# Performance work log

Hardware: AMD Instinct MI355X
Metric: run time of the kernel (lower is better)

Reference implementation:

```python
import jax, jax.numpy as jnp
import numpy as np
import math

H = 5120        # hidden_size
NH = 32         # num heads
HD = H // NH    # head_dim = 160
B = 1
S = 2048
TRAIN_SEQLEN = 8192
BASE = 10000.0


def _rotary_cos_sin(seq_len):
    # Eval-mode RotaryEmbedding: seq_len clamped to training_seqlen, NTK alpha + mscale (logN) scaling.
    eff = max(seq_len, TRAIN_SEQLEN)
    scale = eff / TRAIN_SEQLEN
    mscale = 1.0 if scale <= 1.0 else 0.1 * math.log(scale) + 1.0
    ntk_alpha = max(2 ** math.ceil(math.log(eff / 4096, 2) + 1) - 1, 1)
    base = BASE * ntk_alpha ** (HD / (HD - 2))
    inv_freq = 1.0 / base ** (np.arange(0, HD, 2, dtype=np.float64) / HD)
    t = np.arange(eff, dtype=np.float64)
    freqs = np.outer(t, inv_freq)              # [eff, HD/2]
    emb = np.concatenate([freqs, freqs], axis=-1)  # [eff, HD]
    cos = (mscale * np.cos(emb))[:seq_len].astype(np.float32)
    sin = (mscale * np.sin(emb))[:seq_len].astype(np.float32)
    return jnp.asarray(cos), jnp.asarray(sin)


def _rotate_half(x):
    x1, x2 = x[..., : HD // 2], x[..., HD // 2 :]
    return jnp.concatenate([-x2, x1], axis=-1)


def setup_inputs() -> dict:
    key = jax.random.key(0)
    ks = jax.random.split(key, 6)
    hidden_states = jax.random.normal(ks[0], (B, S, H), jnp.float32)
    residual = jax.random.normal(ks[1], (B, S, H), jnp.float32)
    # boolean causal mask, True = masked (matches masked_fill semantics)
    attention_mask = jnp.triu(jnp.ones((S, S), dtype=bool), k=1)[None, None]
    Wq = jax.random.normal(ks[2], (H, H), jnp.float32) * 0.02      # query: Linear(h, h, bias=False)
    Wkv = jax.random.normal(ks[3], (2 * H, H), jnp.float32) * 0.02  # key_value: Linear(h, 2h, bias=False)
    Wd = jax.random.normal(ks[4], (H, H), jnp.float32) * 0.02       # dense: Linear(h, h) with bias
    bd = jnp.zeros((H,), jnp.float32)
    return {
        "hidden_states": hidden_states,
        "residual": residual,
        "attention_mask": attention_mask,
        "Wq": Wq,
        "Wkv": Wkv,
        "Wd": Wd,
        "bd": bd,
    }


def reference(hidden_states, residual, attention_mask, Wq, Wkv, Wd, bd):
    b, s, h = hidden_states.shape
    # QKV projections (torch Linear: y = x @ W.T)
    q = jnp.einsum('bsh,oh->bso', hidden_states, Wq).reshape(b, s, NH, HD)
    kv = jnp.einsum('bsh,oh->bso', hidden_states, Wkv).reshape(b, s, NH, 2 * HD)
    k, v = kv[..., :HD], kv[..., HD:]
    # rotary embedding with logN mscale folded into cos/sin
    cos, sin = _rotary_cos_sin(s)               # [s, HD]
    cos = cos[None, :, None, :]
    sin = sin[None, :, None, :]
    q = q * cos + _rotate_half(q) * sin
    k = k * cos + _rotate_half(k) * sin
    inv_norm = 1.0 / math.sqrt(HD)
    scores = jnp.einsum('bqnd,bknd->bnqk', q, k) * inv_norm   # [b, nh, s, s]
    scores = jnp.where(attention_mask, jnp.finfo(scores.dtype).min, scores)
    probs = jax.nn.softmax(scores, axis=-1)
    # attention_dropout p=0.0 -> identity
    ctx = jnp.einsum('bnqk,bknd->bqnd', probs, v).reshape(b, s, h)
    out = ctx @ Wd.T + bd
    # dropout_add with hidden_dropout=0.0 (eval) -> residual + out
    return residual + out
```

## Files before the change

### kernel.cpp

```cpp
#include <hip/hip_runtime.h>
#include <cmath>

typedef unsigned short u16;
typedef unsigned int   u32;

using bf16x8 = __attribute__((ext_vector_type(8))) short;
using f32x4  = __attribute__((ext_vector_type(4))) float;

#define S_LEN 2048
#define NHEAD 32
#define HDIM  160
#define HID   5120
#define NQKV  15360

__device__ __forceinline__ f32x4 mfma16(bf16x8 a, bf16x8 b, f32x4 c) {
  return __builtin_amdgcn_mfma_f32_16x16x32_bf16(a, b, c, 0, 0, 0);
}

__device__ __forceinline__ u16 f2bf(float f) {
  u32 u = __builtin_bit_cast(u32, f);
  u += 0x7FFFu + ((u >> 16) & 1u);
  return (u16)(u >> 16);
}
__device__ __forceinline__ float bf2f(u16 h) {
  u32 u = ((u32)h) << 16;
  return __builtin_bit_cast(float, u);
}

__device__ __forceinline__ void gload16(const void* g, void* l) {
  __builtin_amdgcn_global_load_lds((const __attribute__((address_space(1))) void*)g,
                                   (__attribute__((address_space(3))) void*)l, 16, 0, 0);
}

__global__ void cvt_all_kernel(const float* __restrict__ hs, const float* __restrict__ Wq,
                               const float* __restrict__ Wkv, const float* __restrict__ Wd,
                               u16* __restrict__ Xb, u16* __restrict__ Wqkvb,
                               u16* __restrict__ Wdb) {
  const int n_hs = S_LEN * HID / 8;
  const int n_q  = HID * HID / 8;
  const int n_kv = 2 * HID * HID / 8;
  const int n_d  = HID * HID / 8;
  const int total = n_hs + n_q + n_kv + n_d;
  for (int i = blockIdx.x * 256 + threadIdx.x; i < total; i += gridDim.x * 256) {
    const float* src; u16* dst; int j = i;
    if (j < n_hs)                { src = hs;  dst = Xb; }
    else if ((j -= n_hs) < n_q)  { src = Wq;  dst = Wqkvb; }
    else if ((j -= n_q) < n_kv)  { src = Wkv; dst = Wqkvb + (size_t)HID * HID; }
    else { j -= n_kv;              src = Wd;  dst = Wdb; }
    float4 a = ((const float4*)src)[(size_t)j * 2];
    float4 b = ((const float4*)src)[(size_t)j * 2 + 1];
    uint4 o;
    o.x = (u32)f2bf(a.x) | ((u32)f2bf(a.y) << 16);
    o.y = (u32)f2bf(a.z) | ((u32)f2bf(a.w) << 16);
    o.z = (u32)f2bf(b.x) | ((u32)f2bf(b.y) << 16);
    o.w = (u32)f2bf(b.z) | ((u32)f2bf(b.w) << 16);
    ((uint4*)dst)[j] = o;
  }
}

__global__ void rope_table_kernel(float2* __restrict__ tab) {
  __shared__ double invf_s[80];
  int tid = threadIdx.x;
  if (tid < 80) {
    double base = 10000.0 * pow(3.0, 160.0 / 158.0);
    invf_s[tid] = pow(base, -((double)(2 * tid)) / 160.0);
  }
  __syncthreads();
  for (int i = blockIdx.x * 256 + tid; i < S_LEN * 80; i += gridDim.x * 256) {
    int s = i / 80, j = i % 80;
    double ang = fmod((double)s * invf_s[j], 6.283185307179586476925287);
    float a = (float)ang;
    tab[i] = make_float2(cosf(a), sinf(a));
  }
}

__global__ void rope_apply2_kernel(const u16* __restrict__ qkv, const float2* __restrict__ tab,
                                   u16* __restrict__ Qr, u16* __restrict__ Kr) {
  const int n = S_LEN * NHEAD * 80;
  int i = blockIdx.x * 256 + threadIdx.x;
  bool isK = i >= n;
  if (isK) i -= n;
  const u16* src = qkv + (isK ? HID : 0);
  int headStride = isK ? 2 * HDIM : HDIM;
  u16* dst = isK ? Kr : Qr;

  int dp = i % 80; int sh = i / 80; int h = sh % NHEAD; int s = sh / NHEAD;
  int d = 2 * dp;
  const u16* row = src + (size_t)s * NQKV + h * headStride;
  u32 q01 = *(const u32*)&row[d];
  u32 p01 = *(const u32*)&row[d < 80 ? d + 80 : d - 80];
  int j = (d < 80) ? d : d - 80;
  float2 cs0 = tab[s * 80 + j];
  float2 cs1 = tab[s * 80 + j + 1];
  float q0 = bf2f((u16)(q01 & 0xffff)), q1 = bf2f((u16)(q01 >> 16));
  float p0 = bf2f((u16)(p01 & 0xffff)), p1 = bf2f((u16)(p01 >> 16));
  float sgn = (d < 80) ? -1.f : 1.f;
  float o0 = q0 * cs0.x + sgn * p0 * cs0.y;
  float o1 = q1 * cs1.x + sgn * p1 * cs1.y;
  u32 o = (u32)f2bf(o0) | ((u32)f2bf(o1) << 16);
  *(u32*)&dst[((size_t)h * S_LEN + s) * HDIM + d] = o;
}

__global__ void vtrans_kernel(const u16* __restrict__ src, u16* __restrict__ Vt, int rowStride) {
  __shared__ u16 T[HDIM][72];
  int h = blockIdx.y; int s0 = blockIdx.x * 64; int tid = threadIdx.x;
  for (int i = tid; i < 64 * 80; i += 256) {
    int s = i / 80, dp = i % 80;
    u32 v = *(const u32*)&src[(size_t)(s0 + s) * rowStride + h * 320 + 2 * dp];
    T[2 * dp][s]     = (u16)(v & 0xffff);
    T[2 * dp + 1][s] = (u16)(v >> 16);
  }
  __syncthreads();
  for (int i = tid; i < HDIM * 32; i += 256) {
    int d = i / 32, sp = i % 32;
    u32 v = (u32)T[d][2 * sp] | ((u32)T[d][2 * sp + 1] << 16);
    *(u32*)&Vt[((size_t)h * HDIM + d) * S_LEN + s0 + 2 * sp] = v;
  }
}

template<int EPI>
__global__ __launch_bounds__(512, 2) void gemm256(
    const u16* __restrict__ A, const u16* __restrict__ Bm, void* __restrict__ Cout,
    int M, int N, int K, const float* __restrict__ bias, const float* __restrict__ resid)
{
  __shared__ u16 As[2][2][8192];
  __shared__ u16 Bs[2][2][8192];
  int tid = threadIdx.x;
  int w = tid >> 6, l = tid & 63, l15 = l & 15, l4 = l >> 4;
  int wr = w >> 2, wc = w & 3;

  int nbx = gridDim.x;
  int nwg = nbx * gridDim.y;
  int lin = blockIdx.y * nbx + blockIdx.x;
  int cpx = nwg >> 3;
  int swz = (lin & 7) * cpx + (lin >> 3);
  int bm = (swz / nbx) * 256, bn = (swz % nbx) * 256;

  int srow = tid >> 2;
  int scol = ((tid & 3) * 8) ^ ((srow & 8) ? 16 : 0);
  const u16* gAr = A  + (size_t)(bm + srow) * K + scol;
  const u16* gBr = Bm + (size_t)(bn + srow) * K + scol;
  int w512 = w * 512;

  f32x4 acc[8][4];
#pragma unroll
  for (int i = 0; i < 8; i++)
#pragma unroll
    for (int j = 0; j < 4; j++) acc[i][j] = f32x4{0.f, 0.f, 0.f, 0.f};

  int cA = (l4 * 8) ^ ((l15 & 8) ? 16 : 0);
  const int NT = K >> 6;
  int arow = wr * 128;
  int brow = (wc >> 1) * 128 + (wc & 1) * 64;

  auto STA = [&](int kt, int kk) { int p = kt & 1, ko = (kt << 6) + (kk << 5);
    gload16(gAr + ko, &As[p][kk][w512]);
    gload16(gAr + (size_t)128 * K + ko, &As[p][kk][4096 + w512]); };
  auto STB = [&](int kt, int kk) { int p = kt & 1, ko = (kt << 6) + (kk << 5);
    gload16(gBr + ko, &Bs[p][kk][w512]);
    gload16(gBr + (size_t)128 * K + ko, &Bs[p][kk][4096 + w512]); };

  STB(0, 0); STA(0, 0); STB(0, 1); STA(0, 1);
  if (NT > 1) { STB(1, 0); STA(1, 0); STB(1, 1); }
  asm volatile("s_waitcnt vmcnt(6)" ::: "memory");
  __builtin_amdgcn_s_barrier();

  for (int kt = 0; kt < NT; ++kt) {
    int p = kt & 1;
    bf16x8 aF[4], bF0[4], bF1[4];

    if (kt + 1 < NT) STA(kt + 1, 1);
#pragma unroll
    for (int mi = 0; mi < 4; ++mi)
      aF[mi] = *(const bf16x8*)&As[p][0][(arow + mi * 16 + l15) * 32 + cA];
#pragma unroll
    for (int ni = 0; ni < 4; ++ni)
      bF0[ni] = *(const bf16x8*)&Bs[p][0][(brow + ni * 16 + l15) * 32 + cA];
    __builtin_amdgcn_s_barrier();
    __builtin_amdgcn_s_setprio(1);
#pragma unroll
    for (int mi = 0; mi < 4; ++mi)
#pragma unroll
      for (int ni = 0; ni < 4; ++ni)
        acc[mi][ni] = mfma16(aF[mi], bF0[ni], acc[mi][ni]);
    __builtin_amdgcn_s_setprio(0);
    __builtin_amdgcn_s_barrier();

    if (kt + 2 < NT) STB(kt + 2, 0);
#pragma unroll
    for (int mi = 0; mi < 4; ++mi)
      aF[mi] = *(const bf16x8*)&As[p][0][(arow + 64 + mi * 16 + l15) * 32 + cA];
    __builtin_amdgcn_s_barrier();
    __builtin_amdgcn_s_setprio(1);
#pragma unroll
    for (int mi = 0; mi < 4; ++mi)
#pragma unroll
      for (int ni = 0; ni < 4; ++ni)
        acc[4 + mi][ni] = mfma16(aF[mi], bF0[ni], acc[4 + mi][ni]);
    __builtin_amdgcn_s_setprio(0);
    __builtin_amdgcn_s_barrier();

    if (kt + 2 < NT) STA(kt + 2, 0);
#pragma unroll
    for (int mi = 0; mi < 4; ++mi)
      aF[mi] = *(const bf16x8*)&As[p][1][(arow + mi * 16 + l15) * 32 + cA];
#pragma unroll
    for (int ni = 0; ni < 4; ++ni)
      bF1[ni] = *(const bf16x8*)&Bs[p][1][(brow + ni * 16 + l15) * 32 + cA];
    __builtin_amdgcn_s_barrier();
    __builtin_amdgcn_s_setprio(1);
#pragma unroll
    for (int mi = 0; mi < 4; ++mi)
#pragma unroll
      for (int ni = 0; ni < 4; ++ni)
        acc[mi][ni] = mfma16(aF[mi], bF1[ni], acc[mi][ni]);
    __builtin_amdgcn_s_setprio(0);
    __builtin_amdgcn_s_barrier();

    if (kt + 2 < NT) STB(kt + 2, 1);
#pragma unroll
    for (int mi = 0; mi < 4; ++mi)
      aF[mi] = *(const bf16x8*)&As[p][1][(arow + 64 + mi * 16 + l15) * 32 + cA];
    __builtin_amdgcn_s_barrier();
    __builtin_amdgcn_s_setprio(1);
#pragma unroll
    for (int mi = 0; mi < 4; ++mi)
#pragma unroll
      for (int ni = 0; ni < 4; ++ni)
        acc[4 + mi][ni] = mfma16(aF[mi], bF1[ni], acc[4 + mi][ni]);
    __builtin_amdgcn_s_setprio(0);
    if (kt + 2 < NT)      asm volatile("s_waitcnt vmcnt(6)" ::: "memory");
    else if (kt + 1 < NT) asm volatile("s_waitcnt vmcnt(0)" ::: "memory");
    __builtin_amdgcn_s_barrier();
  }

#pragma unroll
  for (int mi = 0; mi < 8; ++mi)
#pragma unroll
    for (int ni = 0; ni < 4; ++ni) {
      int row0 = bm + wr * 128 + mi * 16 + l4 * 4;
      int col  = bn + wc * 64 + ni * 16 + l15;
      if (EPI == 0) {
        u16* C = (u16*)Cout;
#pragma unroll
        for (int r = 0; r < 4; r++) C[(size_t)(row0 + r) * N + col] = f2bf(acc[mi][ni][r]);
      } else {
        float* C = (float*)Cout;
        float b = bias[col];
#pragma unroll
        for (int r = 0; r < 4; r++) {
          size_t idx = (size_t)(row0 + r) * N + col;
          C[idx] = acc[mi][ni][r] + b + resid[idx];
        }
      }
    }
}

template<int EPI>
__global__ __launch_bounds__(256, 2) void gemm_bt(
    const u16* __restrict__ A, const u16* __restrict__ Bm, void* __restrict__ Cout,
    int M, int N, int K, const float* __restrict__ bias, const float* __restrict__ resid)
{
  int tid = threadIdx.x;
  int wv = tid >> 6, l = tid & 63, l15 = l & 15, l4 = l >> 4;
  int nbx = gridDim.x;
  int nwg = nbx * gridDim.y;
  int lin = blockIdx.y * nbx + blockIdx.x;
  int cpx = nwg >> 3;
  int swz = (lin & 7) * cpx + (lin >> 3);
  int bm = (swz / nbx) * 128, bn = (swz % nbx) * 128;

  __shared__ u16 As[128 * 32], Bs[128 * 32];
  f32x4 acc[4][4];
#pragma unroll
  for (int i = 0; i < 4; i++)
#pragma unroll
    for (int j = 0; j < 4; j++) acc[i][j] = f32x4{0.f, 0.f, 0.f, 0.f};

  int wm = (wv >> 1) * 64, wn = (wv & 1) * 64;
  const u16* gA = A + (size_t)(bm + (tid >> 2)) * K + (tid & 3) * 8;
  const u16* gB = Bm + (size_t)(bn + (tid >> 2)) * K + (tid & 3) * 8;
  u16* ldsA = As + wv * 16 * 32;
  u16* ldsB = Bs + wv * 16 * 32;

  for (int k0 = 0; k0 < K; k0 += 32) {
    __syncthreads();
    gload16(gA + k0, ldsA);
    gload16(gA + (size_t)64 * K + k0, ldsA + 64 * 32);
    gload16(gB + k0, ldsB);
    gload16(gB + (size_t)64 * K + k0, ldsB + 64 * 32);
    __syncthreads();
    bf16x8 af[4], bfr[4];
#pragma unroll
    for (int i = 0; i < 4; i++) af[i] = *(const bf16x8*)&As[(wm + i * 16 + l15) * 32 + l4 * 8];
#pragma unroll
    for (int i = 0; i < 4; i++) bfr[i] = *(const bf16x8*)&Bs[(wn + i * 16 + l15) * 32 + l4 * 8];
#pragma unroll
    for (int mi = 0; mi < 4; mi++)
#pragma unroll
      for (int ni = 0; ni < 4; ni++) acc[mi][ni] = mfma16(af[mi], bfr[ni], acc[mi][ni]);
  }

#pragma unroll
  for (int mi = 0; mi < 4; mi++)
#pragma unroll
    for (int ni = 0; ni < 4; ni++) {
      int row0 = bm + wm + mi * 16 + l4 * 4;
      int col  = bn + wn + ni * 16 + l15;
      if (EPI == 0) {
        u16* C = (u16*)Cout;
#pragma unroll
        for (int r = 0; r < 4; r++) C[(size_t)(row0 + r) * N + col] = f2bf(acc[mi][ni][r]);
      } else {
        float* C = (float*)Cout;
        float b = bias[col];
#pragma unroll
        for (int r = 0; r < 4; r++) {
          size_t idx = (size_t)(row0 + r) * N + col;
          C[idx] = acc[mi][ni][r] + b + resid[idx];
        }
      }
    }
}

__global__ __launch_bounds__(512, 4) void attn_kernel(
    const u16* __restrict__ Qr, const u16* __restrict__ Kr,
    const u16* __restrict__ Vt, u16* __restrict__ ctx)
{
  int lin = blockIdx.x;
  int h  = lin & 31;
  int qx = (lin < 256) ? (15 - (lin >> 5)) : ((lin - 256) >> 5);
  int q0 = qx * 128;
  int tid = threadIdx.x;
  int w = tid >> 6, l = tid & 63, l15 = l & 15, l4 = l >> 4;
  int qb = q0 + w * 16;

  __shared__ u16 Ks[64][164];
  __shared__ u16 Vs[160][68];
  __shared__ u16 Plds[8][16][68];

  const u16* Qh = Qr + (size_t)h * S_LEN * HDIM;
  const u16* Kh = Kr + (size_t)h * S_LEN * HDIM;
  const u16* Vh = Vt + (size_t)h * HDIM * S_LEN;

  bf16x8 aQ[5];
#pragma unroll
  for (int kc = 0; kc < 5; kc++)
    aQ[kc] = *(const bf16x8*)&Qh[(size_t)(qb + l15) * HDIM + kc * 32 + l4 * 8];

  f32x4 accO[10];
#pragma unroll
  for (int dt = 0; dt < 10; dt++) accO[dt] = f32x4{0.f, 0.f, 0.f, 0.f};
  float mrun[4], lrun[4];
#pragma unroll
  for (int r = 0; r < 4; r++) { mrun[r] = -1e30f; lrun[r] = 0.f; }

  const float c2 = 0.07905694150420949f * 1.44269504088896f;
  int Tend = 2 * qx + 2;

  {
    uint4 rg[5];
#pragma unroll
    for (int i = 0; i < 5; i++) {
      int u = tid + 512 * i;
      if (u < 1280) { int row = u / 20, c = u % 20;
        rg[i] = *(const uint4*)&Kh[(size_t)row * HDIM + c * 8]; }
      else { int v = u - 1280; int row = v >> 3, c = v & 7;
        rg[i] = *(const uint4*)&Vh[(size_t)row * S_LEN + c * 8]; }
    }
#pragma unroll
    for (int i = 0; i < 5; i++) {
      int u = tid + 512 * i;
      if (u < 1280) { int row = u / 20, c = u % 20; *(uint4*)&Ks[row][c * 8] = rg[i]; }
      else { int v = u - 1280; int row = v >> 3, c = v & 7; *(uint4*)&Vs[row][c * 8] = rg[i]; }
    }
  }
  __syncthreads();

  for (int t = 0; t < Tend; ++t) {
    int k0 = t * 64;
    bool more = (t + 1 < Tend);
    uint4 rg[5];
    if (more) {
      int k1 = k0 + 64;
#pragma unroll
      for (int i = 0; i < 5; i++) {
        int u = tid + 512 * i;
        if (u < 1280) { int row = u / 20, c = u % 20;
          rg[i] = *(const uint4*)&Kh[(size_t)(k1 + row) * HDIM + c * 8]; }
        else { int v = u - 1280; int row = v >> 3, c = v & 7;
          rg[i] = *(const uint4*)&Vh[(size_t)row * S_LEN + k1 + c * 8]; }
      }
    }

    if (k0 <= qb + 15) {
      f32x4 s_[4];
#pragma unroll
      for (int nt = 0; nt < 4; nt++) s_[nt] = f32x4{0.f, 0.f, 0.f, 0.f};

#pragma unroll
      for (int kc = 0; kc < 5; kc++) {
        bf16x8 bK[4];
#pragma unroll
        for (int nt = 0; nt < 4; nt++)
          bK[nt] = *(const bf16x8*)&Ks[nt * 16 + l15][kc * 32 + l4 * 8];
        __builtin_amdgcn_s_setprio(1);
#pragma unroll
        for (int nt = 0; nt < 4; nt++) s_[nt] = mfma16(aQ[kc], bK[nt], s_[nt]);
        __builtin_amdgcn_s_setprio(0);
      }

      if (k0 + 63 > qb) {
#pragma unroll
        for (int nt = 0; nt < 4; nt++)
#pragma unroll
          for (int r = 0; r < 4; r++) {
            int kk = k0 + nt * 16 + l15;
            int qq = qb + l4 * 4 + r;
            if (kk > qq) s_[nt][r] = -1e30f;
          }
      }

      float sf[4];
#pragma unroll
      for (int r = 0; r < 4; r++) {
        float v = fmaxf(fmaxf(s_[0][r], s_[1][r]), fmaxf(s_[2][r], s_[3][r]));
#pragma unroll
        for (int m = 1; m <= 8; m <<= 1) v = fmaxf(v, __shfl_xor(v, m));
        float mnew = fmaxf(mrun[r], v);
        sf[r] = exp2f((mrun[r] - mnew) * c2);
        mrun[r] = mnew;
      }
      float rsum[4] = {0.f, 0.f, 0.f, 0.f};
#pragma unroll
      for (int nt = 0; nt < 4; nt++)
#pragma unroll
        for (int r = 0; r < 4; r++) {
          float p = exp2f((s_[nt][r] - mrun[r]) * c2);
          s_[nt][r] = p;
          rsum[r] += p;
        }
#pragma unroll
      for (int r = 0; r < 4; r++) {
        float v = rsum[r];
#pragma unroll
        for (int m = 1; m <= 8; m <<= 1) v += __shfl_xor(v, m);
        lrun[r] = lrun[r] * sf[r] + v;
      }
#pragma unroll
      for (int dt = 0; dt < 10; dt++)
#pragma unroll
        for (int r = 0; r < 4; r++) accO[dt][r] *= sf[r];
#pragma unroll
      for (int nt = 0; nt < 4; nt++)
#pragma unroll
        for (int r = 0; r < 4; r++)
          Plds[w][l4 * 4 + r][nt * 16 + l15] = f2bf(s_[nt][r]);

#pragma unroll
      for (int kc = 0; kc < 2; kc++) {
        bf16x8 aP = *(const bf16x8*)&Plds[w][l15][kc * 32 + l4 * 8];
        bf16x8 bV[10];
#pragma unroll
        for (int dt = 0; dt < 10; dt++)
          bV[dt] = *(const bf16x8*)&Vs[dt * 16 + l15][kc * 32 + l4 * 8];
        __builtin_amdgcn_s_setprio(1);
#pragma unroll
        for (int dt = 0; dt < 10; dt++)
          accO[dt] = mfma16(aP, bV[dt], accO[dt]);
        __builtin_amdgcn_s_setprio(0);
      }
    }

    __builtin_amdgcn_s_barrier();
    if (more) {
#pragma unroll
      for (int i = 0; i < 5; i++) {
        int u = tid + 512 * i;
        if (u < 1280) { int row = u / 20, c = u % 20; *(uint4*)&Ks[row][c * 8] = rg[i]; }
        else { int v = u - 1280; int row = v >> 3, c = v & 7; *(uint4*)&Vs[row][c * 8] = rg[i]; }
      }
      asm volatile("s_waitcnt lgkmcnt(0)" ::: "memory");
    }
    __builtin_amdgcn_s_barrier();
  }

  float inv[4];
#pragma unroll
  for (int r = 0; r < 4; r++) inv[r] = 1.0f / lrun[r];
#pragma unroll
  for (int dt = 0; dt < 10; dt++)
#pragma unroll
    for (int r = 0; r < 4; r++) {
      int q = qb + l4 * 4 + r;
      ctx[(size_t)q * HID + h * HDIM + dt * 16 + l15] = f2bf(accO[dt][r] * inv[r]);
    }
}

extern "C" void kernel_launch(void* const* d_in, const int* in_sizes, int n_in,
                              void* d_out, int out_size, void* d_ws, size_t ws_size,
                              hipStream_t stream) {
  const float* hs    = (const float*)d_in[0];
  const float* resid = (const float*)d_in[1];
  const float* Wq  = (const float*)d_in[3];
  const float* Wkv = (const float*)d_in[4];
  const float* Wd  = (const float*)d_in[5];
  const float* bd  = (const float*)d_in[6];
  float* out = (float*)d_out;

  char* ws = (char*)d_ws;
  const size_t SH = (size_t)S_LEN * HID;
  u16* Xb     = (u16*)(ws);                        size_t off = SH * 2;
  u16* Wqkvb  = (u16*)(ws + off);                  off += (size_t)3 * HID * HID * 2;
  u16* Wdb    = (u16*)(ws + off);                  off += (size_t)HID * HID * 2;
  u16* QKVraw = (u16*)(ws + off);                  off += (size_t)S_LEN * NQKV * 2;
  u16* Qr     = (u16*)(ws + off);                  off += SH * 2;
  u16* Kr     = (u16*)(ws + off);                  off += SH * 2;
  u16* Vt     = (u16*)(ws + off);                  off += SH * 2;
  u16* ctx    = (u16*)(ws + off);                  off += SH * 2;
  float2* tab = (float2*)(ws + off);               off += (size_t)S_LEN * 80 * 8;

  cvt_all_kernel<<<2048, 256, 0, stream>>>(hs, Wq, Wkv, Wd, Xb, Wqkvb, Wdb);

  rope_table_kernel<<<64, 256, 0, stream>>>(tab);

  gemm256<0><<<dim3(NQKV / 256, S_LEN / 256), 512, 0, stream>>>(
      Xb, Wqkvb, QKVraw, S_LEN, NQKV, HID, nullptr, nullptr);

  rope_apply2_kernel<<<2 * S_LEN * NHEAD * 80 / 256, 256, 0, stream>>>(QKVraw, tab, Qr, Kr);
  vtrans_kernel<<<dim3(S_LEN / 64, NHEAD), 256, 0, stream>>>(QKVraw + HID + HDIM, Vt, NQKV);

  attn_kernel<<<512, 512, 0, stream>>>(Qr, Kr, Vt, ctx);

  gemm_bt<1><<<dim3(HID / 128, S_LEN / 128), 256, 0, stream>>>(
      ctx, Wdb, out, S_LEN, HID, HID, bd, resid);
}
```

Measured before the change: 971.7 us.

## Shrink QKV GEMM tile to 256x128 with simpler double-buffered K=32 pipeline

Reworks the QKV projection GEMM from a 256x256 tile with a two-stage-ahead, four-phase K=64 pipeline to a 256x128 tile with single-stage double buffering over K=32 steps. Each wave now owns a 64x64 output block (16 accumulators instead of 32), and launch bounds request 4 workgroups per CU instead of 2. The intent is more concurrent workgroups and a grid that fills the CUs better. In exchange, data reuse per tile drops, barriers per unit of K work rise, and the prefetch depth is shallower.

```diff
diff --git a/kernel.cpp b/kernel.cpp
--- a/kernel.cpp
+++ b/kernel.cpp
@@ -119,126 +119,80 @@
 }
 
 template<int EPI>
-__global__ __launch_bounds__(512, 2) void gemm256(
+__global__ __launch_bounds__(512, 4) void gemm256(
     const u16* __restrict__ A, const u16* __restrict__ Bm, void* __restrict__ Cout,
     int M, int N, int K, const float* __restrict__ bias, const float* __restrict__ resid)
 {
-  __shared__ u16 As[2][2][8192];
-  __shared__ u16 Bs[2][2][8192];
+  __shared__ u16 As[2][8192];
+  __shared__ u16 Bs[2][4096];
   int tid = threadIdx.x;
   int w = tid >> 6, l = tid & 63, l15 = l & 15, l4 = l >> 4;
-  int wr = w >> 2, wc = w & 3;
+  int wr = w >> 1, wc = w & 1;
 
   int nbx = gridDim.x;
   int nwg = nbx * gridDim.y;
   int lin = blockIdx.y * nbx + blockIdx.x;
   int cpx = nwg >> 3;
   int swz = (lin & 7) * cpx + (lin >> 3);
-  int bm = (swz / nbx) * 256, bn = (swz % nbx) * 256;
+  int bm = (swz / nbx) * 256, bn = (swz % nbx) * 128;
 
   int srow = tid >> 2;
   int scol = ((tid & 3) * 8) ^ ((srow & 8) ? 16 : 0);
-  const u16* gAr = A  + (size_t)(bm + srow) * K + scol;
-  const u16* gBr = Bm + (size_t)(bn + srow) * K + scol;
+  const u16* gA0 = A + (size_t)(bm + srow) * K + scol;
+  const u16* gA1 = gA0 + (size_t)128 * K;
+  const u16* gB  = Bm + (size_t)(bn + srow) * K + scol;
   int w512 = w * 512;
 
-  f32x4 acc[8][4];
-#pragma unroll
-  for (int i = 0; i < 8; i++)
+  f32x4 acc[4][4];
+#pragma unroll
+  for (int i = 0; i < 4; i++)
 #pragma unroll
     for (int j = 0; j < 4; j++) acc[i][j] = f32x4{0.f, 0.f, 0.f, 0.f};
 
   int cA = (l4 * 8) ^ ((l15 & 8) ? 16 : 0);
-  const int NT = K >> 6;
-  int arow = wr * 128;
-  int brow = (wc >> 1) * 128 + (wc & 1) * 64;
-
-  auto STA = [&](int kt, int kk) { int p = kt & 1, ko = (kt << 6) + (kk << 5);
-    gload16(gAr + ko, &As[p][kk][w512]);
-    gload16(gAr + (size_t)128 * K + ko, &As[p][kk][4096 + w512]); };
-  auto STB = [&](int kt, int kk) { int p = kt & 1, ko = (kt << 6) + (kk << 5);
-    gload16(gBr + ko, &Bs[p][kk][w512]);
-    gload16(gBr + (size_t)128 * K + ko, &Bs[p][kk][4096 + w512]); };
-
-  STB(0, 0); STA(0, 0); STB(0, 1); STA(0, 1);
-  if (NT > 1) { STB(1, 0); STA(1, 0); STB(1, 1); }
-  asm volatile("s_waitcnt vmcnt(6)" ::: "memory");
-  __builtin_amdgcn_s_barrier();
-
+  const int NT = K >> 5;
+  int arow = wr * 64;
+  int brow = wc * 64;
+
+  auto STAGE = [&](int kt) { int p = kt & 1, ko = kt << 5;
+    gload16(gA0 + ko, &As[p][w512]);
+    gload16(gA1 + ko, &As[p][4096 + w512]);
+    gload16(gB  + ko, &Bs[p][w512]);
+  };
+
+  STAGE(0);
   for (int kt = 0; kt < NT; ++kt) {
     int p = kt & 1;
-    bf16x8 aF[4], bF0[4], bF1[4];
-
-    if (kt + 1 < NT) STA(kt + 1, 1);
+    if (kt + 1 < NT) {
+      STAGE(kt + 1);
+      asm volatile("s_waitcnt vmcnt(3)" ::: "memory");
+    } else {
+      asm volatile("s_waitcnt vmcnt(0)" ::: "memory");
+    }
+    __builtin_amdgcn_s_barrier();
+
+    bf16x8 aF[4], bF[4];
 #pragma unroll
     for (int mi = 0; mi < 4; ++mi)
-      aF[mi] = *(const bf16x8*)&As[p][0][(arow + mi * 16 + l15) * 32 + cA];
+      aF[mi] = *(const bf16x8*)&As[p][(arow + mi * 16 + l15) * 32 + cA];
 #pragma unroll
     for (int ni = 0; ni < 4; ++ni)
-      bF0[ni] = *(const bf16x8*)&Bs[p][0][(brow + ni * 16 + l15) * 32 + cA];
-    __builtin_amdgcn_s_barrier();
+      bF[ni] = *(const bf16x8*)&Bs[p][(brow + ni * 16 + l15) * 32 + cA];
     __builtin_amdgcn_s_setprio(1);
 #pragma unroll
     for (int mi = 0; mi < 4; ++mi)
 #pragma unroll
       for (int ni = 0; ni < 4; ++ni)
-        acc[mi][ni] = mfma16(aF[mi], bF0[ni], acc[mi][ni]);
+        acc[mi][ni] = mfma16(aF[mi], bF[ni], acc[mi][ni]);
     __builtin_amdgcn_s_setprio(0);
     __builtin_amdgcn_s_barrier();
-
-    if (kt + 2 < NT) STB(kt + 2, 0);
-#pragma unroll
-    for (int mi = 0; mi < 4; ++mi)
-      aF[mi] = *(const bf16x8*)&As[p][0][(arow + 64 + mi * 16 + l15) * 32 + cA];
-    __builtin_amdgcn_s_barrier();
-    __builtin_amdgcn_s_setprio(1);
-#pragma unroll
-    for (int mi = 0; mi < 4; ++mi)
-#pragma unroll
-      for (int ni = 0; ni < 4; ++ni)
-        acc[4 + mi][ni] = mfma16(aF[mi], bF0[ni], acc[4 + mi][ni]);
-    __builtin_amdgcn_s_setprio(0);
-    __builtin_amdgcn_s_barrier();
-
-    if (kt + 2 < NT) STA(kt + 2, 0);
-#pragma unroll
-    for (int mi = 0; mi < 4; ++mi)
-      aF[mi] = *(const bf16x8*)&As[p][1][(arow + mi * 16 + l15) * 32 + cA];
-#pragma unroll
-    for (int ni = 0; ni < 4; ++ni)
-      bF1[ni] = *(const bf16x8*)&Bs[p][1][(brow + ni * 16 + l15) * 32 + cA];
-    __builtin_amdgcn_s_barrier();
-    __builtin_amdgcn_s_setprio(1);
-#pragma unroll
-    for (int mi = 0; mi < 4; ++mi)
-#pragma unroll
-      for (int ni = 0; ni < 4; ++ni)
-        acc[mi][ni] = mfma16(aF[mi], bF1[ni], acc[mi][ni]);
-    __builtin_amdgcn_s_setprio(0);
-    __builtin_amdgcn_s_barrier();
-
-    if (kt + 2 < NT) STB(kt + 2, 1);
-#pragma unroll
-    for (int mi = 0; mi < 4; ++mi)
-      aF[mi] = *(const bf16x8*)&As[p][1][(arow + 64 + mi * 16 + l15) * 32 + cA];
-    __builtin_amdgcn_s_barrier();
-    __builtin_amdgcn_s_setprio(1);
-#pragma unroll
-    for (int mi = 0; mi < 4; ++mi)
-#pragma unroll
-      for (int ni = 0; ni < 4; ++ni)
-        acc[4 + mi][ni] = mfma16(aF[mi], bF1[ni], acc[4 + mi][ni]);
-    __builtin_amdgcn_s_setprio(0);
-    if (kt + 2 < NT)      asm volatile("s_waitcnt vmcnt(6)" ::: "memory");
-    else if (kt + 1 < NT) asm volatile("s_waitcnt vmcnt(0)" ::: "memory");
-    __builtin_amdgcn_s_barrier();
-  }
-
-#pragma unroll
-  for (int mi = 0; mi < 8; ++mi)
+  }
+
+#pragma unroll
+  for (int mi = 0; mi < 4; ++mi)
 #pragma unroll
     for (int ni = 0; ni < 4; ++ni) {
-      int row0 = bm + wr * 128 + mi * 16 + l4 * 4;
+      int row0 = bm + wr * 64 + mi * 16 + l4 * 4;
       int col  = bn + wc * 64 + ni * 16 + l15;
       if (EPI == 0) {
         u16* C = (u16*)Cout;
@@ -524,7 +478,7 @@
 
   rope_table_kernel<<<64, 256, 0, stream>>>(tab);
 
-  gemm256<0><<<dim3(NQKV / 256, S_LEN / 256), 512, 0, stream>>>(
+  gemm256<0><<<dim3(NQKV / 128, S_LEN / 256), 512, 0, stream>>>(
       Xb, Wqkvb, QKVraw, S_LEN, NQKV, HID, nullptr, nullptr);
 
   rope_apply2_kernel<<<2 * S_LEN * NHEAD * 80 / 256, 256, 0, stream>>>(QKVraw, tab, Qr, Kr);
```

After: 947.2 us. 2.5% less time.
